# Optimization experiments

Measured on AMD Instinct MI355X. Metric: run time of the kernel, lower is better.

Reference implementation:

```python
import jax, jax.numpy as jnp
import numpy as np

N = 100000
E = 3200000
NEG_SLOPE = 0.2  # PyG GATConv default


def gat_layer(x, src, dst, W, a_src, a_dst, b, heads, out_ch, concat):
    # per-node linear transform, split into heads: [N, H, C]
    h = (x @ W).reshape(N, heads, out_ch)
    # per-node attention logits: [N, H]
    al_src = jnp.sum(h * a_src, axis=-1)
    al_dst = jnp.sum(h * a_dst, axis=-1)
    # per-edge attention coefficient (x_j = source, x_i = target): [E, H]
    e = jax.nn.leaky_relu(al_src[src] + al_dst[dst], NEG_SLOPE)
    # segment softmax over incoming edges of each destination node
    m = jax.ops.segment_max(e, dst, num_segments=N)
    e = jnp.exp(e - m[dst])
    denom = jax.ops.segment_sum(e, dst, num_segments=N)
    alpha = e / (denom[dst] + 1e-16)
    # weighted message aggregation: scatter-add over dst
    msg = h[src] * alpha[..., None]  # [E, H, C]
    out = jax.ops.segment_sum(msg, dst, num_segments=N)  # [N, H, C]
    out = out.reshape(N, heads * out_ch) if concat else out.mean(axis=1)
    return out + b


def setup_inputs() -> dict:
    key = jax.random.key(0)
    ks = jax.random.split(key, 11)
    return {
        "x": jax.random.normal(ks[0], (N, 2), dtype=jnp.float32),
        "edge_index": jax.random.randint(ks[1], (2, E), 0, N, dtype=jnp.int64),
        "edge_attr": jax.random.normal(ks[2], (E, 1), dtype=jnp.float32),
        "W1": jax.random.normal(ks[3], (2, 32), dtype=jnp.float32) * 0.5,
        "att_src1": jax.random.normal(ks[4], (4, 8), dtype=jnp.float32) * 0.3,
        "att_dst1": jax.random.normal(ks[5], (4, 8), dtype=jnp.float32) * 0.3,
        "b1": jnp.zeros((32,), dtype=jnp.float32),
        "W2": jax.random.normal(ks[6], (32, 2), dtype=jnp.float32) * 0.2,
        "att_src2": jax.random.normal(ks[7], (1, 2), dtype=jnp.float32) * 0.3,
        "att_dst2": jax.random.normal(ks[8], (1, 2), dtype=jnp.float32) * 0.3,
        "b2": jnp.zeros((2,), dtype=jnp.float32),
    }


def reference(x, edge_index, edge_attr, W1, att_src1, att_dst1, b1, W2, att_src2, att_dst2, b2):
    # add self-loops (PyG GATConv default add_self_loops=True)
    loops = jnp.arange(N, dtype=edge_index.dtype)
    src = jnp.concatenate([edge_index[0], loops])
    dst = jnp.concatenate([edge_index[1], loops])
    h = gat_layer(x, src, dst, W1, att_src1, att_dst1, b1, heads=4, out_ch=8, concat=True)
    h = jax.nn.elu(h)
    out = gat_layer(h, src, dst, W2, att_src2, att_dst2, b2, heads=1, out_ch=2, concat=False)
    return out
```

## Files before the change

### kernel.cpp

```cpp
#include <hip/hip_runtime.h>
#include <hip/hip_bf16.h>
#include <math.h>

#define NEG_SLOPE 0.2f
#define BK_BITS 9
#define BK (1 << BK_BITS)
#define SBITS 17
#define SMASK ((1 << SBITS) - 1)
#define CAP 20480
#define HRSTRIDE (CAP + 1024)

__device__ __forceinline__ float lrelu(float x) { return x > 0.f ? x : NEG_SLOPE * x; }

__global__ void init_bcur(int* __restrict__ bcur, int NB) {
    int i = threadIdx.x;
    if (i < NB) bcur[i] = i * CAP;
}

__global__ __launch_bounds__(256) void bucket_scatter(const int* __restrict__ src,
                                                      const int* __restrict__ dst,
                                                      int* __restrict__ bcur,
                                                      int* __restrict__ pairs, int E) {
    __shared__ int cnt[256], sc[256], off[256], cur[256], gbase[256];
    __shared__ int lpair[4096];
    __shared__ unsigned char lbkt[4096];
    int t = threadIdx.x;
    cnt[t] = 0;
    __syncthreads();

    int E4 = E >> 2;
    const int4* src4 = (const int4*)src;
    const int4* dst4 = (const int4*)dst;
    int base4 = blockIdx.x * 1024;
    int4 d4[4], s4[4];
    bool val[4];
#pragma unroll
    for (int k = 0; k < 4; k++) {
        int i4 = base4 + k * 256 + t;
        val[k] = (i4 < E4);
        if (val[k]) {
            d4[k] = dst4[i4];
            s4[k] = src4[i4];
            atomicAdd(&cnt[d4[k].x >> BK_BITS], 1);
            atomicAdd(&cnt[d4[k].y >> BK_BITS], 1);
            atomicAdd(&cnt[d4[k].z >> BK_BITS], 1);
            atomicAdd(&cnt[d4[k].w >> BK_BITS], 1);
        }
    }
    int dt = -1, st = 0;
    if (blockIdx.x == gridDim.x - 1) {
        int e = (E4 << 2) + t;
        if (e < E) { dt = dst[e]; st = src[e]; atomicAdd(&cnt[dt >> BK_BITS], 1); }
    }
    __syncthreads();

    sc[t] = cnt[t];
    __syncthreads();
    for (int o = 1; o < 256; o <<= 1) {
        int u = (t >= o) ? sc[t - o] : 0;
        __syncthreads();
        sc[t] += u;
        __syncthreads();
    }
    int excl = (t == 0) ? 0 : sc[t - 1];
    off[t] = excl;
    cur[t] = excl;
    if (cnt[t] > 0) gbase[t] = atomicAdd(&bcur[t], cnt[t]);
    __syncthreads();
    int total = sc[255];

#pragma unroll
    for (int k = 0; k < 4; k++) {
        if (val[k]) {
            int b, slot;
            b = d4[k].x >> BK_BITS; slot = atomicAdd(&cur[b], 1);
            lpair[slot] = ((d4[k].x & (BK - 1)) << SBITS) | s4[k].x; lbkt[slot] = (unsigned char)b;
            b = d4[k].y >> BK_BITS; slot = atomicAdd(&cur[b], 1);
            lpair[slot] = ((d4[k].y & (BK - 1)) << SBITS) | s4[k].y; lbkt[slot] = (unsigned char)b;
            b = d4[k].z >> BK_BITS; slot = atomicAdd(&cur[b], 1);
            lpair[slot] = ((d4[k].z & (BK - 1)) << SBITS) | s4[k].z; lbkt[slot] = (unsigned char)b;
            b = d4[k].w >> BK_BITS; slot = atomicAdd(&cur[b], 1);
            lpair[slot] = ((d4[k].w & (BK - 1)) << SBITS) | s4[k].w; lbkt[slot] = (unsigned char)b;
        }
    }
    if (dt >= 0) {
        int b = dt >> BK_BITS;
        int slot = atomicAdd(&cur[b], 1);
        lpair[slot] = ((dt & (BK - 1)) << SBITS) | st; lbkt[slot] = (unsigned char)b;
    }
    __syncthreads();

    for (int i = t; i < total; i += 256) {
        int b = lbkt[i];
        pairs[gbase[b] + (i - off[b])] = lpair[i];
    }
}

__global__ __launch_bounds__(1024) void csr_build(const int* __restrict__ pairs,
                                                  const int* __restrict__ bcur,
                                                  int* __restrict__ row_deg,
                                                  int* __restrict__ csr_src, int N) {
    int bh = blockIdx.x;
    int b = bh >> 1, half = bh & 1;
    int t = threadIdx.x;
    int lo = b * CAP, hi = bcur[b];
    int dbase0 = (b << BK_BITS) + (half << 8);
    int ndst = min(256, N - dbase0);
    if (ndst <= 0) return;
    int base2 = bh * HRSTRIDE;
    __shared__ int cnt[256];
    __shared__ int sc[256];
    __shared__ int cur[256];
    if (t < 256) cnt[t] = 0;
    __syncthreads();
    for (int i = lo + t; i < hi; i += 1024) {
        int dl = pairs[i] >> SBITS;
        if ((dl >> 8) == half) atomicAdd(&cnt[dl & 255], 1);
    }
    __syncthreads();
    int d0 = 0, a0 = 0;
    if (t < 256) {
        d0 = (t < ndst) ? cnt[t] + 1 : 0;
        a0 = (d0 + 3) & ~3;
        sc[t] = a0;
    }
    __syncthreads();
    for (int o = 1; o < 256; o <<= 1) {
        int u = 0;
        if (t < 256 && t >= o) u = sc[t - o];
        __syncthreads();
        if (t < 256) sc[t] += u;
        __syncthreads();
    }
    if (t < ndst) {
        int excl = (t == 0) ? 0 : sc[t - 1];
        row_deg[dbase0 + t] = (excl << 16) | d0;
        csr_src[base2 + excl] = dbase0 + t;
        for (int k = d0; k < a0; k++) csr_src[base2 + excl + k] = dbase0 + t;
        cur[t] = excl + 1;
    }
    __syncthreads();
    for (int i = lo + t; i < hi; i += 1024) {
        int p = pairs[i];
        int dl = p >> SBITS;
        if ((dl >> 8) == half) {
            int pos = atomicAdd(&cur[dl & 255], 1);
            csr_src[base2 + pos] = p & SMASK;
        }
    }
}

__global__ __launch_bounds__(256) void agg1_dstlane(
        const int* __restrict__ row_deg, const int* __restrict__ csr_src,
        const float2* __restrict__ x2,
        const float* __restrict__ W1, const float* __restrict__ asrc,
        const float* __restrict__ adst, const float* __restrict__ b1,
        const float* __restrict__ W2, const float* __restrict__ as2,
        const float* __restrict__ ad2,
        float2* __restrict__ h2, float* __restrict__ al2d, int N) {
    __shared__ float sW[64], sB[32], sW2[64], sP[4], sQ[4], sPd[4], sQd[4], sA2[4];
    int t = threadIdx.x;
    if (t < 64) { sW[t] = W1[t]; sW2[t] = W2[t]; }
    if (t < 32) sB[t] = b1[t];
    if (t < 2) { sA2[t] = as2[t]; sA2[2 + t] = ad2[t]; }
    if (t < 4) {
        float P = 0.f, Q = 0.f, Pd = 0.f, Qd = 0.f;
#pragma unroll
        for (int k = 0; k < 8; k++) {
            int c = t * 8 + k;
            float a = asrc[c], ad_ = adst[c];
            float w0 = W1[c], w1 = W1[32 + c];
            P += w0 * a; Q += w1 * a;
            Pd += w0 * ad_; Qd += w1 * ad_;
        }
        sP[t] = P; sQ[t] = Q; sPd[t] = Pd; sQd[t] = Qd;
    }
    __syncthreads();

    int tid = blockIdx.x * blockDim.x + t;
    int n = tid >> 2;
    int q = tid & 3;
    if (n >= N) return;
    int rd = row_deg[n];
    int row = (n >> 8) * HRSTRIDE + (rd >> 16);
    int deg = rd & 0xFFFF;

    float2 xd = x2[n];
    float P[4], Q[4], ald[4];
#pragma unroll
    for (int h = 0; h < 4; h++) {
        P[h] = sP[h]; Q[h] = sQ[h];
        ald[h] = xd.x * sPd[h] + xd.y * sQd[h];
    }

    float Sw[4] = {0.f, 0.f, 0.f, 0.f};
    float S0[4] = {0.f, 0.f, 0.f, 0.f};
    float S1[4] = {0.f, 0.f, 0.f, 0.f};
    for (int j = q * 4; j < deg; j += 16) {
        int4 s4 = *(const int4*)(csr_src + row + j);
        float2 xs[4];
        xs[0] = x2[s4.x]; xs[1] = x2[s4.y]; xs[2] = x2[s4.z]; xs[3] = x2[s4.w];
#pragma unroll
        for (int k = 0; k < 4; k++) {
            bool live = (j + k < deg);
#pragma unroll
            for (int h = 0; h < 4; h++) {
                float e = lrelu(fmaf(xs[k].x, P[h], fmaf(xs[k].y, Q[h], ald[h])));
                float w = __expf(fminf(e, 80.f));
                w = live ? w : 0.f;
                Sw[h] += w;
                S0[h] += w * xs[k].x;
                S1[h] += w * xs[k].y;
            }
        }
    }
#pragma unroll
    for (int o = 1; o <= 2; o <<= 1) {
#pragma unroll
        for (int h = 0; h < 4; h++) {
            Sw[h] += __shfl_xor(Sw[h], o);
            S0[h] += __shfl_xor(S0[h], o);
            S1[h] += __shfl_xor(S1[h], o);
        }
    }
    if (q != 0) return;

    float r[4];
#pragma unroll
    for (int h = 0; h < 4; h++) r[h] = 1.f / (Sw[h] + 1e-16f);
    float h20 = 0.f, h21 = 0.f;
#pragma unroll
    for (int c = 0; c < 32; c++) {
        int h = c >> 3;
        float outc = (sW[c] * S0[h] + sW[32 + c] * S1[h]) * r[h];
        float v2 = outc + sB[c];
        v2 = v2 > 0.f ? v2 : __expf(v2) - 1.f;
        h20 = fmaf(v2, sW2[2 * c], h20);
        h21 = fmaf(v2, sW2[2 * c + 1], h21);
    }
    h2[n] = make_float2(h20, h21);
    al2d[n] = h20 * sA2[2] + h21 * sA2[3];
}

__global__ __launch_bounds__(256) void agg2_dstlane(
        const int* __restrict__ row_deg, const int* __restrict__ csr_src,
        const float* __restrict__ al2d, const float2* __restrict__ h2,
        const float* __restrict__ as2, const float* __restrict__ b2,
        float2* __restrict__ out, int N) {
    int tid = blockIdx.x * blockDim.x + threadIdx.x;
    int n = tid >> 2;
    int q = tid & 3;
    if (n >= N) return;
    int rd = row_deg[n];
    int row = (n >> 8) * HRSTRIDE + (rd >> 16);
    int deg = rd & 0xFFFF;
    float ald = al2d[n];
    float a0 = as2[0], a1 = as2[1];

    float wsum = 0.f, ax = 0.f, ay = 0.f;
    for (int j = q * 4; j < deg; j += 16) {
        int4 s4 = *(const int4*)(csr_src + row + j);
        float2 hv[4];
        hv[0] = h2[s4.x]; hv[1] = h2[s4.y]; hv[2] = h2[s4.z]; hv[3] = h2[s4.w];
#pragma unroll
        for (int k = 0; k < 4; k++) {
            float e = lrelu(fmaf(hv[k].x, a0, fmaf(hv[k].y, a1, ald)));
            float w = __expf(fminf(e, 80.f));
            w = (j + k < deg) ? w : 0.f;
            wsum += w;
            ax = fmaf(w, hv[k].x, ax);
            ay = fmaf(w, hv[k].y, ay);
        }
    }
#pragma unroll
    for (int o = 1; o <= 2; o <<= 1) {
        wsum += __shfl_xor(wsum, o);
        ax += __shfl_xor(ax, o);
        ay += __shfl_xor(ay, o);
    }
    if (q != 0) return;
    float inv = 1.f / (wsum + 1e-16f);
    out[n] = make_float2(ax * inv + b2[0], ay * inv + b2[1]);
}

extern "C" void kernel_launch(void* const* d_in, const int* in_sizes, int n_in,
                              void* d_out, int out_size, void* d_ws, size_t ws_size,
                              hipStream_t stream) {
    const float* x     = (const float*)d_in[0];
    const int*   eidx  = (const int*)d_in[1];
    const float* W1    = (const float*)d_in[3];
    const float* asrc1 = (const float*)d_in[4];
    const float* adst1 = (const float*)d_in[5];
    const float* b1    = (const float*)d_in[6];
    const float* W2    = (const float*)d_in[7];
    const float* asrc2 = (const float*)d_in[8];
    const float* adst2 = (const float*)d_in[9];
    const float* b2    = (const float*)d_in[10];

    const int N = in_sizes[0] / 2;
    const int E = in_sizes[1] / 2;
    const int* src = eidx;
    const int* dst = eidx + E;
    const int NB = (N + BK - 1) >> BK_BITS;
    const int NH = 2 * NB;

    float* w = (float*)d_ws;
    float2* h2    = (float2*)w;
    float*  al2d  = w + 2 * (size_t)N;
    int* ip       = (int*)(w + 3 * (size_t)N);
    int* row_deg  = ip;
    int* bcur     = ip + (size_t)N;
    int* pairs    = ip + (size_t)N + 200;
    int* csr_src  = pairs + (size_t)NB * CAP;

    const int B = 256;
    int E4 = E >> 2;
    int gS = (E4 + 1023) / 1024;
    int gL4 = (4 * N + B - 1) / B;

    init_bcur<<<1, B, 0, stream>>>(bcur, NB);
    bucket_scatter<<<gS, B, 0, stream>>>(src, dst, bcur, pairs, E);
    csr_build<<<NH, 1024, 0, stream>>>(pairs, bcur, row_deg, csr_src, N);

    agg1_dstlane<<<gL4, B, 0, stream>>>(row_deg, csr_src, (const float2*)x,
                                        W1, asrc1, adst1, b1, W2, asrc2, adst2,
                                        h2, al2d, N);
    agg2_dstlane<<<gL4, B, 0, stream>>>(row_deg, csr_src, al2d, h2, asrc2, b2,
                                        (float2*)d_out, N);
}
```

Baseline: 188.5 us.

## Fuse CSR build with first-layer aggregation using LDS-resident CSR rows

Merges the csr_build and agg1 kernels so that each 1024-thread block builds the CSR for its 256 destinations and then aggregates them right away. The block reads source indices from an LDS copy of the CSR instead of re-reading global memory. Pairs are cached in registers (PPT per thread) so the bucket is read from global memory only once for both the count and scatter passes. This removes one launch and a global round trip, but uses 40KB LDS plus many registers. It also cuts parallelism in agg1 to 256 of 1024 threads per block with 4 lanes per node.

```diff
diff --git a/kernel.cpp b/kernel.cpp
--- a/kernel.cpp
+++ b/kernel.cpp
@@ -9,6 +9,8 @@
 #define SMASK ((1 << SBITS) - 1)
 #define CAP 20480
 #define HRSTRIDE (CAP + 1024)
+#define LCAP 10240
+#define PPT 17
 
 __device__ __forceinline__ float lrelu(float x) { return x > 0.f ? x : NEG_SLOPE * x; }
 
@@ -96,10 +98,15 @@
     }
 }
 
-__global__ __launch_bounds__(1024) void csr_build(const int* __restrict__ pairs,
-                                                  const int* __restrict__ bcur,
-                                                  int* __restrict__ row_deg,
-                                                  int* __restrict__ csr_src, int N) {
+__global__ __launch_bounds__(1024) void csr_agg1(
+        const int* __restrict__ pairs, const int* __restrict__ bcur,
+        const float2* __restrict__ x2,
+        const float* __restrict__ W1, const float* __restrict__ asrc,
+        const float* __restrict__ adst, const float* __restrict__ b1,
+        const float* __restrict__ W2, const float* __restrict__ as2,
+        const float* __restrict__ ad2,
+        int* __restrict__ row_deg, int* __restrict__ csr_src,
+        float2* __restrict__ h2, float* __restrict__ al2d, int N) {
     int bh = blockIdx.x;
     int b = bh >> 1, half = bh & 1;
     int t = threadIdx.x;
@@ -108,61 +115,14 @@
     int ndst = min(256, N - dbase0);
     if (ndst <= 0) return;
     int base2 = bh * HRSTRIDE;
-    __shared__ int cnt[256];
-    __shared__ int sc[256];
-    __shared__ int cur[256];
-    if (t < 256) cnt[t] = 0;
-    __syncthreads();
-    for (int i = lo + t; i < hi; i += 1024) {
-        int dl = pairs[i] >> SBITS;
-        if ((dl >> 8) == half) atomicAdd(&cnt[dl & 255], 1);
-    }
-    __syncthreads();
-    int d0 = 0, a0 = 0;
-    if (t < 256) {
-        d0 = (t < ndst) ? cnt[t] + 1 : 0;
-        a0 = (d0 + 3) & ~3;
-        sc[t] = a0;
-    }
-    __syncthreads();
-    for (int o = 1; o < 256; o <<= 1) {
-        int u = 0;
-        if (t < 256 && t >= o) u = sc[t - o];
-        __syncthreads();
-        if (t < 256) sc[t] += u;
-        __syncthreads();
-    }
-    if (t < ndst) {
-        int excl = (t == 0) ? 0 : sc[t - 1];
-        row_deg[dbase0 + t] = (excl << 16) | d0;
-        csr_src[base2 + excl] = dbase0 + t;
-        for (int k = d0; k < a0; k++) csr_src[base2 + excl + k] = dbase0 + t;
-        cur[t] = excl + 1;
-    }
-    __syncthreads();
-    for (int i = lo + t; i < hi; i += 1024) {
-        int p = pairs[i];
-        int dl = p >> SBITS;
-        if ((dl >> 8) == half) {
-            int pos = atomicAdd(&cur[dl & 255], 1);
-            csr_src[base2 + pos] = p & SMASK;
-        }
-    }
-}
-
-__global__ __launch_bounds__(256) void agg1_dstlane(
-        const int* __restrict__ row_deg, const int* __restrict__ csr_src,
-        const float2* __restrict__ x2,
-        const float* __restrict__ W1, const float* __restrict__ asrc,
-        const float* __restrict__ adst, const float* __restrict__ b1,
-        const float* __restrict__ W2, const float* __restrict__ as2,
-        const float* __restrict__ ad2,
-        float2* __restrict__ h2, float* __restrict__ al2d, int N) {
-    __shared__ float sW[64], sB[32], sW2[64], sP[4], sQ[4], sPd[4], sQd[4], sA2[4];
-    int t = threadIdx.x;
+
+    __shared__ int lcsr[LCAP];
+    __shared__ int cnt[256], sc[256], cur[256];
+    __shared__ float sW[64], sB[32], sW2[64], sP[4], sQ[4], sPd[4], sQd[4], sA2[2];
+
     if (t < 64) { sW[t] = W1[t]; sW2[t] = W2[t]; }
     if (t < 32) sB[t] = b1[t];
-    if (t < 2) { sA2[t] = as2[t]; sA2[2 + t] = ad2[t]; }
+    if (t < 2) sA2[t] = ad2[t];
     if (t < 4) {
         float P = 0.f, Q = 0.f, Pd = 0.f, Qd = 0.f;
 #pragma unroll
@@ -175,15 +135,83 @@
         }
         sP[t] = P; sQ[t] = Q; sPd[t] = Pd; sQd[t] = Qd;
     }
-    __syncthreads();
-
-    int tid = blockIdx.x * blockDim.x + t;
-    int n = tid >> 2;
-    int q = tid & 3;
-    if (n >= N) return;
-    int rd = row_deg[n];
-    int row = (n >> 8) * HRSTRIDE + (rd >> 16);
-    int deg = rd & 0xFFFF;
+    if (t < 256) cnt[t] = 0;
+    __syncthreads();
+
+    int myp[PPT];
+#pragma unroll
+    for (int k = 0; k < PPT; k++) {
+        int i = lo + t + k * 1024;
+        int p = (i < hi) ? pairs[i] : -1;
+        myp[k] = p;
+        if (p >= 0) {
+            int dl = p >> SBITS;
+            if ((dl >> 8) == half) atomicAdd(&cnt[dl & 255], 1);
+        }
+    }
+    for (int i = lo + t + PPT * 1024; i < hi; i += 1024) {
+        int dl = pairs[i] >> SBITS;
+        if ((dl >> 8) == half) atomicAdd(&cnt[dl & 255], 1);
+    }
+    __syncthreads();
+
+    int d0 = 0, a0 = 0;
+    if (t < 256) {
+        d0 = (t < ndst) ? cnt[t] + 1 : 0;
+        a0 = (d0 + 3) & ~3;
+        sc[t] = a0;
+    }
+    __syncthreads();
+    for (int o = 1; o < 256; o <<= 1) {
+        int u = (t < 256 && t >= o) ? sc[t - o] : 0;
+        __syncthreads();
+        if (t < 256) sc[t] += u;
+        __syncthreads();
+    }
+    if (t < 256) cnt[t] = d0;
+    if (t < ndst) {
+        int excl = t ? sc[t - 1] : 0;
+        row_deg[dbase0 + t] = (excl << 16) | d0;
+        lcsr[excl] = dbase0 + t;
+        csr_src[base2 + excl] = dbase0 + t;
+        for (int k = d0; k < a0; k++) {
+            lcsr[excl + k] = dbase0 + t;
+            csr_src[base2 + excl + k] = dbase0 + t;
+        }
+        cur[t] = excl + 1;
+    }
+    __syncthreads();
+
+#pragma unroll
+    for (int k = 0; k < PPT; k++) {
+        int p = myp[k];
+        if (p >= 0) {
+            int dl = p >> SBITS;
+            if ((dl >> 8) == half) {
+                int pos = atomicAdd(&cur[dl & 255], 1);
+                int s = p & SMASK;
+                lcsr[pos] = s;
+                csr_src[base2 + pos] = s;
+            }
+        }
+    }
+    for (int i = lo + t + PPT * 1024; i < hi; i += 1024) {
+        int p = pairs[i];
+        int dl = p >> SBITS;
+        if ((dl >> 8) == half) {
+            int pos = atomicAdd(&cur[dl & 255], 1);
+            int s = p & SMASK;
+            lcsr[pos] = s;
+            csr_src[base2 + pos] = s;
+        }
+    }
+    __syncthreads();
+
+    int i = t >> 2, q = t & 3;
+    if (i >= ndst) return;
+    int n = dbase0 + i;
+    int deg = cnt[i];
+    int rowl = i ? sc[i - 1] : 0;
 
     float2 xd = x2[n];
     float P[4], Q[4], ald[4];
@@ -192,12 +220,11 @@
         P[h] = sP[h]; Q[h] = sQ[h];
         ald[h] = xd.x * sPd[h] + xd.y * sQd[h];
     }
-
     float Sw[4] = {0.f, 0.f, 0.f, 0.f};
     float S0[4] = {0.f, 0.f, 0.f, 0.f};
     float S1[4] = {0.f, 0.f, 0.f, 0.f};
     for (int j = q * 4; j < deg; j += 16) {
-        int4 s4 = *(const int4*)(csr_src + row + j);
+        int4 s4 = *(const int4*)(lcsr + rowl + j);
         float2 xs[4];
         xs[0] = x2[s4.x]; xs[1] = x2[s4.y]; xs[2] = x2[s4.z]; xs[3] = x2[s4.w];
 #pragma unroll
@@ -239,7 +266,7 @@
         h21 = fmaf(v2, sW2[2 * c + 1], h21);
     }
     h2[n] = make_float2(h20, h21);
-    al2d[n] = h20 * sA2[2] + h21 * sA2[3];
+    al2d[n] = h20 * sA2[0] + h21 * sA2[1];
 }
 
 __global__ __launch_bounds__(256) void agg2_dstlane(
@@ -320,11 +347,9 @@
 
     init_bcur<<<1, B, 0, stream>>>(bcur, NB);
     bucket_scatter<<<gS, B, 0, stream>>>(src, dst, bcur, pairs, E);
-    csr_build<<<NH, 1024, 0, stream>>>(pairs, bcur, row_deg, csr_src, N);
-
-    agg1_dstlane<<<gL4, B, 0, stream>>>(row_deg, csr_src, (const float2*)x,
-                                        W1, asrc1, adst1, b1, W2, asrc2, adst2,
-                                        h2, al2d, N);
+    csr_agg1<<<NH, 1024, 0, stream>>>(pairs, bcur, (const float2*)x,
+                                      W1, asrc1, adst1, b1, W2, asrc2, adst2,
+                                      row_deg, csr_src, h2, al2d, N);
     agg2_dstlane<<<gL4, B, 0, stream>>>(row_deg, csr_src, al2d, h2, asrc2, b2,
                                         (float2*)d_out, N);
 }
```

Measured after the change: 189.9 us. About the same (+0.8%).
